# Optimization experiments

Hardware: AMD Instinct MI355X
Metric: run time of the kernel (lower is better)

## Reference

```python
import jax, jax.numpy as jnp
import numpy as np

N, E = 50000, 800000
IN_DIM, C = 128, 32
H_STD, H_REP = 3, 1
EE_HID, EE_OUT = 32, 16
NEG_SLOPE = 0.2


def setup_inputs() -> dict:
    key = jax.random.key(0)
    ks = jax.random.split(key, 24)
    rn = lambda k, shape, scale: jax.random.normal(k, shape, jnp.float32) * scale
    inp = {
        "x": rn(ks[0], (N, IN_DIM), 1.0),
        "edge_features_raw": jax.random.uniform(ks[1], (E, 7), jnp.float32),
        "edge_index": jax.random.randint(ks[2], (2, E), 0, N, dtype=jnp.int32),
        "same_type_mask": jax.random.randint(ks[3], (E,), 0, 2, dtype=jnp.int32) > 0,
        # edge encoder MLP 7 -> 32 -> 16
        "ee_w1": rn(ks[4], (7, EE_HID), 7 ** -0.5),
        "ee_b1": jnp.zeros((EE_HID,), jnp.float32),
        "ee_w2": rn(ks[5], (EE_HID, EE_OUT), EE_HID ** -0.5),
        "ee_b2": jnp.zeros((EE_OUT,), jnp.float32),
        # standard GATv2 (3 heads)
        "wl_s": rn(ks[6], (IN_DIM, H_STD * C), IN_DIM ** -0.5),
        "bl_s": jnp.zeros((H_STD * C,), jnp.float32),
        "wr_s": rn(ks[7], (IN_DIM, H_STD * C), IN_DIM ** -0.5),
        "br_s": jnp.zeros((H_STD * C,), jnp.float32),
        "we_s": rn(ks[8], (EE_OUT, H_STD * C), EE_OUT ** -0.5),
        "att_s": rn(ks[9], (H_STD, C), C ** -0.5),
        "bias_s": jnp.zeros((H_STD * C,), jnp.float32),
        # repulsion GATv2 (1 head)
        "wl_r": rn(ks[10], (IN_DIM, H_REP * C), IN_DIM ** -0.5),
        "bl_r": jnp.zeros((H_REP * C,), jnp.float32),
        "wr_r": rn(ks[11], (IN_DIM, H_REP * C), IN_DIM ** -0.5),
        "br_r": jnp.zeros((H_REP * C,), jnp.float32),
        "we_r": rn(ks[12], (EE_OUT, H_REP * C), EE_OUT ** -0.5),
        "att_r": rn(ks[13], (H_REP, C), C ** -0.5),
        "bias_r": jnp.zeros((H_REP * C,), jnp.float32),
    }
    return inp


def _gatv2(x, src, dst, edge_attr, edge_mask, wl, bl, wr, br, we, att, bias, n, h, c):
    """GATv2Conv (eval mode). src/dst already include self loops; edge_mask masks
    attention (-inf) for edges excluded from this head's graph."""
    xl = (x @ wl + bl).reshape(n, h, c)            # source transform
    xr = (x @ wr + br).reshape(n, h, c)            # target transform
    ef = (edge_attr @ we).reshape(-1, h, c)        # edge transform
    msg = xl[src] + xr[dst] + ef                   # [E', H, C]
    score = jnp.einsum('ehc,hc->eh', jax.nn.leaky_relu(msg, NEG_SLOPE), att)
    score = jnp.where(edge_mask[:, None], score, -jnp.inf)
    smax = jax.ops.segment_max(score, dst, num_segments=n)   # every node has a self loop
    a = jnp.exp(score - smax[dst])                 # masked edges -> 0
    denom = jax.ops.segment_sum(a, dst, num_segments=n)
    a = a / denom[dst]
    out = jax.ops.segment_sum(a[:, :, None] * xl[src], dst, num_segments=n)
    return out.reshape(n, h * c) + bias


def reference(x, edge_features_raw, ee_w1, ee_b1, ee_w2, ee_b2,
              wl_s, bl_s, wr_s, br_s, we_s, att_s, bias_s,
              wl_r, bl_r, wr_r, br_r, we_r, att_r, bias_r,
              edge_index, same_type_mask):
    n = x.shape[0]
    # edge encoder MLP
    ea = jax.nn.relu(edge_features_raw @ ee_w1 + ee_b1) @ ee_w2 + ee_b2  # [E, 16]
    src, dst = edge_index[0], edge_index[1]
    loop = jnp.arange(n, dtype=src.dtype)
    src_f = jnp.concatenate([src, loop])
    dst_f = jnp.concatenate([dst, loop])
    # standard conv: self-loop edge_attr = mean over all edges
    ea_std = jnp.concatenate([ea, jnp.broadcast_to(ea.mean(0), (n, ea.shape[1]))], 0)
    mask_std = jnp.ones(src_f.shape[0], bool)
    h_std = _gatv2(x, src_f, dst_f, ea_std, mask_std,
                   wl_s, bl_s, wr_s, br_s, we_s, att_s, bias_s, n, H_STD, C)
    # repulsion conv on same-type edge subset (+ self loops); loop attr = masked mean
    m = same_type_mask.astype(ea.dtype)
    ea_loop_rep = (ea * m[:, None]).sum(0) / jnp.maximum(m.sum(), 1.0)
    ea_rep = jnp.concatenate([ea, jnp.broadcast_to(ea_loop_rep, (n, ea.shape[1]))], 0)
    mask_rep = jnp.concatenate([same_type_mask, jnp.ones(n, bool)])
    h_rep = _gatv2(x, src_f, dst_f, ea_rep, mask_rep,
                   wl_r, bl_r, wr_r, br_r, we_r, att_r, bias_r, n, H_REP, C)
    return jnp.concatenate([h_std, h_rep], axis=-1)  # [N, (3+1)*32]
```

## Files before the change

### kernel.cpp

```cpp
#include <hip/hip_runtime.h>
#include <hip/hip_bf16.h>
#include <cstdint>

#define IN_DIM 128
#define OUT_STD 96
#define OUT_REP 32
#define OUT_ALL 128
#define NEG_SLOPE 0.2f
#define EE_BLOCKS 512
#define LOG2E 1.4426950408889634f

typedef _Float16 h2 __attribute__((ext_vector_type(2)));
typedef _Float16 f16x8 __attribute__((ext_vector_type(8)));
typedef float f32x4 __attribute__((ext_vector_type(4)));

template <int CTRL>
__device__ __forceinline__ float dpp_add(float v)
{
    int x = __builtin_amdgcn_update_dpp(0, __float_as_int(v), CTRL, 0xf, 0xf, true);
    return v + __int_as_float(x);
}
__device__ __forceinline__ float grp32_sum(float v)
{
    v = dpp_add<0xB1>(v);
    v = dpp_add<0x4E>(v);
    v = dpp_add<0x141>(v);
    v = dpp_add<0x140>(v);
    int x = __builtin_amdgcn_ds_swizzle(__float_as_int(v), 0x401F);
    return v + __int_as_float(x);
}

__device__ __forceinline__ int detect_mask_fl(const void* mraw, int nprobe, int* sfl)
{
    int t = threadIdx.x;
    const unsigned char* mb = (const unsigned char*)mraw;
    int anyGT1 = 0, any123 = 0;
    for (int i = t; i < nprobe; i += 256) {
        unsigned char b = mb[i];
        if (b > 1) anyGT1 = 1;
        if ((i & 3) && b) any123 = 1;
    }
    anyGT1 = __any(anyGT1);
    any123 = __any(any123);
    if (t == 0) *sfl = 0;
    __syncthreads();
    if ((t & 63) == 0) atomicOr(sfl, (anyGT1 ? 2 : 0) | (any123 ? 1 : 0));
    __syncthreads();
    int v = *sfl;
    return (v & 2) ? 2 : ((v & 1) ? 0 : 1);
}

__device__ __forceinline__ bool mask_at(const void* m, int fl, int e)
{
    if (fl == 1) return ((const int*)m)[e] != 0;
    if (fl == 2) return ((const float*)m)[e] != 0.f;
    return ((const unsigned char*)m)[e] != 0;
}

__global__ __launch_bounds__(256) void initpack(
    const float* __restrict__ wls, const float* __restrict__ wrs,
    const float* __restrict__ wlr, const float* __restrict__ wrr,
    const float* __restrict__ bls, const float* __restrict__ brs,
    const float* __restrict__ blr, const float* __restrict__ brr,
    int* __restrict__ deg, float* __restrict__ sums,
    _Float16* __restrict__ Wh, float* __restrict__ biasp, int N)
{
    int gid = blockIdx.x * 256 + threadIdx.x;
    int gs = gridDim.x * 256;
    for (int i = gid; i < N; i += gs) deg[i] = 0;
    if (gid < 64) sums[gid] = 0.f;
    for (int i = gid; i < 128 * 256; i += gs) {
        int j = i & 255, k = i >> 8;
        float v;
        if (j < 96)       v = wls[k * 96 + j];
        else if (j < 128) v = wlr[k * 32 + (j - 96)];
        else if (j < 224) v = wrs[k * 96 + (j - 128)];
        else              v = wrr[k * 32 + (j - 224)];
        Wh[j * 128 + k] = (_Float16)v;
    }
    if (gid < 256) {
        float b;
        if (gid < 96)       b = bls[gid];
        else if (gid < 128) b = blr[gid - 96];
        else if (gid < 224) b = brs[gid - 128];
        else                b = brr[gid - 224];
        biasp[gid] = b;
    }
}

__global__ __launch_bounds__(256) void edge_enc(
    const float* __restrict__ raw, const int* __restrict__ ei,
    const void* __restrict__ mraw, int nprobe,
    const float* __restrict__ w1, const float* __restrict__ b1,
    const float* __restrict__ w2, const float* __restrict__ b2,
    _Float16* __restrict__ ea, int* __restrict__ deg, float* __restrict__ sums, int E)
{
    __shared__ float sW1[224];
    __shared__ float sB1[32];
    __shared__ float sW2[512];
    __shared__ float sB2[16];
    __shared__ float sraw[256 * 7];
    __shared__ float red[33][4];
    __shared__ int sfl;
    int t = threadIdx.x;
    int fl = detect_mask_fl(mraw, nprobe, &sfl);
    if (t < 224) sW1[t] = w1[t];
    if (t < 32)  sB1[t] = b1[t];
    for (int i = t; i < 512; i += 256) sW2[i] = w2[i];
    if (t < 16)  sB2[t] = b2[t];
    __syncthreads();

    float accs[16], accm[16], cnt = 0.f;
#pragma unroll
    for (int j = 0; j < 16; ++j) { accs[j] = 0.f; accm[j] = 0.f; }

    for (int base = blockIdx.x * 256; base < E; base += gridDim.x * 256) {
        int nh = E - base; if (nh > 256) nh = 256;
        __syncthreads();
        for (int i = t; i < nh * 7; i += 256) sraw[i] = raw[(size_t)base * 7 + i];
        __syncthreads();
        int e = base + t;
        if (e < E) {
            float r[7];
#pragma unroll
            for (int k = 0; k < 7; ++k) r[k] = sraw[t * 7 + k];
            float o[16];
#pragma unroll
            for (int j = 0; j < 16; ++j) o[j] = sB2[j];
#pragma unroll
            for (int jh = 0; jh < 32; ++jh) {
                float hv = sB1[jh];
#pragma unroll
                for (int k = 0; k < 7; ++k) hv += r[k] * sW1[k * 32 + jh];
                hv = hv > 0.f ? hv : 0.f;
#pragma unroll
                for (int j = 0; j < 16; ++j) o[j] += hv * sW2[jh * 16 + j];
            }
            union { h2 h[8]; uint4 u[2]; } pk;
#pragma unroll
            for (int j = 0; j < 8; ++j) pk.h[j] = h2{(_Float16)o[2 * j], (_Float16)o[2 * j + 1]};
            uint4* dst = (uint4*)(ea + (size_t)e * 16);
            dst[0] = pk.u[0];
            dst[1] = pk.u[1];
            atomicAdd(&deg[ei[E + e]], 1);
            float mk = mask_at(mraw, fl, e) ? 1.f : 0.f;
#pragma unroll
            for (int j = 0; j < 16; ++j) { accs[j] += o[j]; accm[j] += o[j] * mk; }
            cnt += mk;
        }
    }

    int wv = t >> 6, ln = t & 63;
#pragma unroll
    for (int j = 0; j < 16; ++j) {
        float v = accs[j], vm = accm[j];
#pragma unroll
        for (int off = 32; off; off >>= 1) {
            v  += __shfl_xor(v, off, 64);
            vm += __shfl_xor(vm, off, 64);
        }
        if (ln == 0) { red[j][wv] = v; red[16 + j][wv] = vm; }
    }
    {
        float c = cnt;
#pragma unroll
        for (int off = 32; off; off >>= 1) c += __shfl_xor(c, off, 64);
        if (ln == 0) red[32][wv] = c;
    }
    __syncthreads();
    if (t < 33) {
        float v = red[t][0] + red[t][1] + red[t][2] + red[t][3];
        atomicAdd(&sums[t], v);
    }
}

__global__ __launch_bounds__(256) void scan1(const int* __restrict__ deg, int* __restrict__ part, int n)
{
    __shared__ int sm[256];
    int i = blockIdx.x * 256 + threadIdx.x;
    sm[threadIdx.x] = (i < n) ? deg[i] : 0;
    __syncthreads();
    for (int s = 128; s; s >>= 1) {
        if (threadIdx.x < s) sm[threadIdx.x] += sm[threadIdx.x + s];
        __syncthreads();
    }
    if (threadIdx.x == 0) part[blockIdx.x] = sm[0];
}

__global__ __launch_bounds__(256) void scan23p(
    const int* __restrict__ deg, const int* __restrict__ part,
    int* __restrict__ row_ofs, int* __restrict__ cursor,
    int n, int E,
    const float* __restrict__ we_s, const float* __restrict__ we_r,
    const float* __restrict__ att_s, const float* __restrict__ att_r,
    const float* __restrict__ bias_s, const float* __restrict__ bias_r,
    const float* __restrict__ sums,
    _Float16* __restrict__ wpk, float* __restrict__ eflv,
    float* __restrict__ attvv, float* __restrict__ biasvv)
{
    __shared__ int sm[256];
    __shared__ int spre;
    int t = threadIdx.x, b = blockIdx.x;
    sm[t] = (t < b) ? part[t] : 0;
    __syncthreads();
    for (int s = 128; s; s >>= 1) {
        if (t < s) sm[t] += sm[t + s];
        __syncthreads();
    }
    if (t == 0) spre = sm[0];
    __syncthreads();
    int prefix = spre;
    __syncthreads();
    int i = b * 256 + t;
    int v = (i < n) ? deg[i] : 0;
    sm[t] = v;
    __syncthreads();
    for (int o = 1; o < 256; o <<= 1) {
        int add = (t >= o) ? sm[t - o] : 0;
        __syncthreads();
        sm[t] += add;
        __syncthreads();
    }
    int excl = sm[t] - v + prefix;
    if (i < n) { row_ofs[i] = excl; cursor[i] = excl; }
    if (b == 0 && t == 0) row_ofs[n] = E;

    if (b == 0 && t < 128) {
        bool is_std = t < OUT_STD;
        int fc = is_std ? t : (t - OUT_STD);
        const float* wsrc = is_std ? we_s : we_r;
        int ldw = is_std ? OUT_STD : OUT_REP;
        const float* sp = is_std ? sums : (sums + 16);
        float c = sums[32]; c = c < 1.f ? 1.f : c;
        float scl = is_std ? (1.f / (float)E) : (1.f / c);
        float efl = 0.f;
#pragma unroll
        for (int k = 0; k < 16; ++k) {
            float v2 = wsrc[k * ldw + fc];
            wpk[t * 16 + k] = (_Float16)v2;
            efl += sp[k] * scl * v2;
        }
        eflv[t] = efl;
        attvv[t] = (is_std ? att_s[t] : att_r[fc]) * LOG2E;
        biasvv[t] = is_std ? bias_s[t] : bias_r[fc];
    }
}

__global__ __launch_bounds__(256) void csr_fill(const int* __restrict__ ei, int* __restrict__ cursor,
                                                const void* __restrict__ mraw, int nprobe,
                                                uint2* __restrict__ csr, int E)
{
    __shared__ int sfl;
    int fl = detect_mask_fl(mraw, nprobe, &sfl);
    int e = blockIdx.x * 256 + threadIdx.x;
    if (e < E) {
        int s = ei[e];
        int d = ei[E + e];
        int slot = atomicAdd(&cursor[d], 1);
        unsigned int v = (unsigned int)e;
        if (mask_at(mraw, fl, e)) v |= 0x80000000u;
        csr[slot] = make_uint2(v, (unsigned int)s);
    }
}

#define NG_BM 64
__global__ __launch_bounds__(256) void node_gemm(
    const float* __restrict__ x, const _Float16* __restrict__ Wh,
    const float* __restrict__ biasp,
    _Float16* __restrict__ XLh, float* __restrict__ XR, int n)
{
    __shared__ __align__(16) _Float16 Ash[64 * 128];
    __shared__ __align__(16) _Float16 Bsh[256 * 128];
    __shared__ float bsh[256];
    int tid = threadIdx.x;
    int m0 = blockIdx.x * NG_BM;

    bsh[tid] = biasp[tid];

    for (int c = tid; c < 64 * 16; c += 256) {
        int row = c >> 4, kc = c & 15;
        int gr = m0 + row;
        float4 a0 = make_float4(0.f, 0.f, 0.f, 0.f), a1 = a0;
        if (gr < n) {
            const float4* xp = (const float4*)(x + (size_t)gr * 128 + kc * 8);
            a0 = xp[0]; a1 = xp[1];
        }
        _Float16* dst = Ash + row * 128 + (kc ^ (row & 7)) * 8;
        dst[0] = (_Float16)a0.x; dst[1] = (_Float16)a0.y;
        dst[2] = (_Float16)a0.z; dst[3] = (_Float16)a0.w;
        dst[4] = (_Float16)a1.x; dst[5] = (_Float16)a1.y;
        dst[6] = (_Float16)a1.z; dst[7] = (_Float16)a1.w;
    }
    for (int c = tid; c < 256 * 16; c += 256) {
        int col = c >> 4, kc = c & 15;
        uint4 v = *(const uint4*)(Wh + col * 128 + kc * 8);
        *(uint4*)(Bsh + col * 128 + (kc ^ (col & 7)) * 8) = v;
    }
    __syncthreads();

    int wave = tid >> 6;
    int lane = tid & 63;
    int l16  = lane & 15;
    int lk   = lane >> 4;

    f32x4 acc0, acc1, acc2, acc3, acc4, acc5, acc6, acc7;
    f32x4 acc8, acc9, acc10, acc11, acc12, acc13, acc14, acc15;
    acc0 = acc1 = acc2 = acc3 = acc4 = acc5 = acc6 = acc7 = f32x4{0.f, 0.f, 0.f, 0.f};
    acc8 = acc9 = acc10 = acc11 = acc12 = acc13 = acc14 = acc15 = f32x4{0.f, 0.f, 0.f, 0.f};

#pragma unroll
    for (int kk = 0; kk < 4; ++kk) {
        int arow = wave * 16 + l16;
        f16x8 afrag = *(const f16x8*)(Ash + arow * 128 + ((kk * 4 + lk) ^ (arow & 7)) * 8);
#define BF(nt) (*(const f16x8*)(Bsh + (nt * 16 + l16) * 128 + ((kk * 4 + lk) ^ ((nt * 16 + l16) & 7)) * 8))
        acc0  = __builtin_amdgcn_mfma_f32_16x16x32_f16(afrag, BF(0),  acc0,  0, 0, 0);
        acc1  = __builtin_amdgcn_mfma_f32_16x16x32_f16(afrag, BF(1),  acc1,  0, 0, 0);
        acc2  = __builtin_amdgcn_mfma_f32_16x16x32_f16(afrag, BF(2),  acc2,  0, 0, 0);
        acc3  = __builtin_amdgcn_mfma_f32_16x16x32_f16(afrag, BF(3),  acc3,  0, 0, 0);
        acc4  = __builtin_amdgcn_mfma_f32_16x16x32_f16(afrag, BF(4),  acc4,  0, 0, 0);
        acc5  = __builtin_amdgcn_mfma_f32_16x16x32_f16(afrag, BF(5),  acc5,  0, 0, 0);
        acc6  = __builtin_amdgcn_mfma_f32_16x16x32_f16(afrag, BF(6),  acc6,  0, 0, 0);
        acc7  = __builtin_amdgcn_mfma_f32_16x16x32_f16(afrag, BF(7),  acc7,  0, 0, 0);
        acc8  = __builtin_amdgcn_mfma_f32_16x16x32_f16(afrag, BF(8),  acc8,  0, 0, 0);
        acc9  = __builtin_amdgcn_mfma_f32_16x16x32_f16(afrag, BF(9),  acc9,  0, 0, 0);
        acc10 = __builtin_amdgcn_mfma_f32_16x16x32_f16(afrag, BF(10), acc10, 0, 0, 0);
        acc11 = __builtin_amdgcn_mfma_f32_16x16x32_f16(afrag, BF(11), acc11, 0, 0, 0);
        acc12 = __builtin_amdgcn_mfma_f32_16x16x32_f16(afrag, BF(12), acc12, 0, 0, 0);
        acc13 = __builtin_amdgcn_mfma_f32_16x16x32_f16(afrag, BF(13), acc13, 0, 0, 0);
        acc14 = __builtin_amdgcn_mfma_f32_16x16x32_f16(afrag, BF(14), acc14, 0, 0, 0);
        acc15 = __builtin_amdgcn_mfma_f32_16x16x32_f16(afrag, BF(15), acc15, 0, 0, 0);
#undef BF
    }

#define STORE_ACC(nt, accv)                                             \
    {                                                                   \
        int col = nt * 16 + l16;                                        \
        float bv = bsh[col];                                            \
        _Pragma("unroll")                                               \
        for (int r = 0; r < 4; ++r) {                                   \
            int row = m0 + wave * 16 + lk * 4 + r;                      \
            if (row < n) {                                              \
                float v = accv[r] + bv;                                 \
                if (col < 128) XLh[(size_t)row * 128 + col] = (_Float16)v; \
                else           XR[(size_t)row * 128 + (col - 128)] = v; \
            }                                                           \
        }                                                               \
    }
    STORE_ACC(0, acc0)   STORE_ACC(1, acc1)   STORE_ACC(2, acc2)   STORE_ACC(3, acc3)
    STORE_ACC(4, acc4)   STORE_ACC(5, acc5)   STORE_ACC(6, acc6)   STORE_ACC(7, acc7)
    STORE_ACC(8, acc8)   STORE_ACC(9, acc9)   STORE_ACC(10, acc10) STORE_ACC(11, acc11)
    STORE_ACC(12, acc12) STORE_ACC(13, acc13) STORE_ACC(14, acc14) STORE_ACC(15, acc15)
#undef STORE_ACC
}

__device__ __forceinline__ void edge_sc(
    const _Float16* __restrict__ XLh, const _Float16* __restrict__ ea,
    const uint2* __restrict__ csr, int pp, int f, bool is_std,
    float xr_n, float attv,
    h2 w0, h2 w1, h2 w2, h2 w3, h2 w4, h2 w5, h2 w6, h2 w7,
    float& s, float& x)
{
    uint2 pk = csr[pp];
    int e = __builtin_amdgcn_readfirstlane((int)(pk.x & 0x7fffffffu));
    bool act = is_std || (pk.x & 0x80000000u);
    int src = __builtin_amdgcn_readfirstlane((int)pk.y);
    x = (float)XLh[(size_t)src * 128 + f];
    union { uint4 u[2]; h2 h[8]; } pe;
    const uint4* eap = (const uint4*)(ea + (size_t)e * 16);
    pe.u[0] = eap[0]; pe.u[1] = eap[1];
    float efv = x + xr_n;
    efv = __builtin_amdgcn_fdot2(pe.h[0], w0, efv, false);
    efv = __builtin_amdgcn_fdot2(pe.h[1], w1, efv, false);
    efv = __builtin_amdgcn_fdot2(pe.h[2], w2, efv, false);
    efv = __builtin_amdgcn_fdot2(pe.h[3], w3, efv, false);
    efv = __builtin_amdgcn_fdot2(pe.h[4], w4, efv, false);
    efv = __builtin_amdgcn_fdot2(pe.h[5], w5, efv, false);
    efv = __builtin_amdgcn_fdot2(pe.h[6], w6, efv, false);
    efv = __builtin_amdgcn_fdot2(pe.h[7], w7, efv, false);
    float lk = fmaxf(efv, NEG_SLOPE * efv);
    float sv = grp32_sum(lk * attv);
    s = act ? sv : -INFINITY;
}

__global__ __launch_bounds__(128, 4) void gat_main(
    const _Float16* __restrict__ XLh, const float* __restrict__ XR,
    const _Float16* __restrict__ ea, const uint2* __restrict__ csr,
    const int* __restrict__ row_ofs,
    const _Float16* __restrict__ wpk, const float* __restrict__ eflv,
    const float* __restrict__ attvv, const float* __restrict__ biasvv,
    float* __restrict__ out, int n)
{
    int node = blockIdx.x;
    int f = threadIdx.x;
    bool is_std = f < OUT_STD;

    union { uint4 u; h2 h[4]; } c0, c1;
    const uint4* wp = (const uint4*)(wpk + (size_t)f * 16);
    c0.u = wp[0]; c1.u = wp[1];
    h2 w0 = c0.h[0], w1 = c0.h[1], w2 = c0.h[2], w3 = c0.h[3];
    h2 w4 = c1.h[0], w5 = c1.h[1], w6 = c1.h[2], w7 = c1.h[3];

    float efl   = eflv[f];
    float attv  = attvv[f];
    float biasv = biasvv[f];

    float xl_n = (float)XLh[(size_t)node * 128 + f];
    float xr_n = XR[(size_t)node * 128 + f];

    float msg = xl_n + xr_n + efl;
    float lk0 = fmaxf(msg, NEG_SLOPE * msg);
    float m = grp32_sum(lk0 * attv);
    float denom = 1.f, acc = xl_n;

    int p0 = row_ofs[node], p1 = row_ofs[node + 1];
    int p = p0;
    for (; p + 8 <= p1; p += 8) {
        float s0, s1, s2, s3, s4, s5, s6, s7;
        float x0, x1, x2, x3, x4, x5, x6, x7;
        edge_sc(XLh, ea, csr, p + 0, f, is_std, xr_n, attv, w0, w1, w2, w3, w4, w5, w6, w7, s0, x0);
        edge_sc(XLh, ea, csr, p + 1, f, is_std, xr_n, attv, w0, w1, w2, w3, w4, w5, w6, w7, s1, x1);
        edge_sc(XLh, ea, csr, p + 2, f, is_std, xr_n, attv, w0, w1, w2, w3, w4, w5, w6, w7, s2, x2);
        edge_sc(XLh, ea, csr, p + 3, f, is_std, xr_n, attv, w0, w1, w2, w3, w4, w5, w6, w7, s3, x3);
        edge_sc(XLh, ea, csr, p + 4, f, is_std, xr_n, attv, w0, w1, w2, w3, w4, w5, w6, w7, s4, x4);
        edge_sc(XLh, ea, csr, p + 5, f, is_std, xr_n, attv, w0, w1, w2, w3, w4, w5, w6, w7, s5, x5);
        edge_sc(XLh, ea, csr, p + 6, f, is_std, xr_n, attv, w0, w1, w2, w3, w4, w5, w6, w7, s6, x6);
        edge_sc(XLh, ea, csr, p + 7, f, is_std, xr_n, attv, w0, w1, w2, w3, w4, w5, w6, w7, s7, x7);

        float mn = fmaxf(m, fmaxf(fmaxf(fmaxf(s0, s1), fmaxf(s2, s3)),
                                  fmaxf(fmaxf(s4, s5), fmaxf(s6, s7))));
        float r  = exp2f(m - mn);
        float q0 = exp2f(s0 - mn), q1 = exp2f(s1 - mn);
        float q2 = exp2f(s2 - mn), q3 = exp2f(s3 - mn);
        float q4 = exp2f(s4 - mn), q5 = exp2f(s5 - mn);
        float q6 = exp2f(s6 - mn), q7 = exp2f(s7 - mn);
        denom = denom * r + (((q0 + q1) + (q2 + q3)) + ((q4 + q5) + (q6 + q7)));
        acc   = acc * r + (((q0 * x0 + q1 * x1) + (q2 * x2 + q3 * x3))
                         + ((q4 * x4 + q5 * x5) + (q6 * x6 + q7 * x7)));
        m = mn;
    }
    for (; p < p1; ++p) {
        float s8, x8;
        edge_sc(XLh, ea, csr, p, f, is_std, xr_n, attv, w0, w1, w2, w3, w4, w5, w6, w7, s8, x8);
        float mn = fmaxf(m, s8);
        float r  = exp2f(m - mn);
        float q  = exp2f(s8 - mn);
        denom = denom * r + q;
        acc   = acc * r + q * x8;
        m = mn;
    }
    out[(size_t)node * OUT_ALL + f] = acc / denom + biasv;
}

extern "C" void kernel_launch(void* const* d_in, const int* in_sizes, int n_in,
                              void* d_out, int out_size, void* d_ws, size_t ws_size,
                              hipStream_t stream)
{
    const float* x    = (const float*)d_in[0];
    const float* raw  = (const float*)d_in[1];
    const int*   ei   = (const int*)d_in[2];
    const void*  mask_raw = d_in[3];
    const float* ee_w1 = (const float*)d_in[4];
    const float* ee_b1 = (const float*)d_in[5];
    const float* ee_w2 = (const float*)d_in[6];
    const float* ee_b2 = (const float*)d_in[7];
    const float* wl_s = (const float*)d_in[8];
    const float* bl_s = (const float*)d_in[9];
    const float* wr_s = (const float*)d_in[10];
    const float* br_s = (const float*)d_in[11];
    const float* we_s = (const float*)d_in[12];
    const float* att_s = (const float*)d_in[13];
    const float* bias_s = (const float*)d_in[14];
    const float* wl_r = (const float*)d_in[15];
    const float* bl_r = (const float*)d_in[16];
    const float* wr_r = (const float*)d_in[17];
    const float* br_r = (const float*)d_in[18];
    const float* we_r = (const float*)d_in[19];
    const float* att_r = (const float*)d_in[20];
    const float* bias_r = (const float*)d_in[21];

    const int N = in_sizes[0] / IN_DIM;
    const int E = in_sizes[1] / 7;

    char* w = (char*)d_ws;
    size_t off = 0;
    auto carve = [&](size_t bytes) {
        void* p = w + off;
        off = (off + bytes + 255) & ~(size_t)255;
        return p;
    };
    _Float16* XLh  = (_Float16*)carve((size_t)N * 128 * 2);
    float* XR      = (float*)carve((size_t)N * 128 * 4);
    _Float16* ea   = (_Float16*)carve((size_t)E * 16 * 2);
    uint2* csr     = (uint2*)carve((size_t)E * 8);
    int*   row_ofs = (int*)carve((size_t)(N + 1) * 4);
    int*   cursor  = (int*)carve((size_t)N * 4);
    int*   deg     = (int*)carve((size_t)N * 4);
    int*   part    = (int*)carve(1024);
    float* sums    = (float*)carve(256);
    _Float16* Wh   = (_Float16*)carve((size_t)256 * 128 * 2);
    float* biasp   = (float*)carve(1024);
    _Float16* wpk  = (_Float16*)carve((size_t)128 * 16 * 2);
    float* eflv    = (float*)carve(512);
    float* attvv   = (float*)carve(512);
    float* biasvv  = (float*)carve(512);
    (void)ws_size; (void)n_in; (void)out_size;

    int ebl = (E + 255) / 256;
    int nbl = (N + 255) / 256;
    int nprobe = E < 4096 ? E : 4096;
    int eebl = ebl < EE_BLOCKS ? ebl : EE_BLOCKS;

    initpack<<<160, 256, 0, stream>>>(wl_s, wr_s, wl_r, wr_r, bl_s, br_s, bl_r, br_r,
                                      deg, sums, Wh, biasp, N);
    edge_enc<<<eebl, 256, 0, stream>>>(raw, ei, mask_raw, nprobe,
                                       ee_w1, ee_b1, ee_w2, ee_b2, ea, deg, sums, E);
    scan1<<<nbl, 256, 0, stream>>>(deg, part, N);
    scan23p<<<nbl, 256, 0, stream>>>(deg, part, row_ofs, cursor, N, E,
                                     we_s, we_r, att_s, att_r, bias_s, bias_r, sums,
                                     wpk, eflv, attvv, biasvv);
    csr_fill<<<ebl, 256, 0, stream>>>(ei, cursor, mask_raw, nprobe, csr, E);
    node_gemm<<<(N + NG_BM - 1) / NG_BM, 256, 0, stream>>>(x, Wh, biasp, XLh, XR, N);
    gat_main<<<N, 128, 0, stream>>>(XLh, XR, ea, csr, row_ofs,
                                    wpk, eflv, attvv, biasvv,
                                    (float*)d_out, N);
}
```

Baseline: 285.4 us.

## Fuse edge encoder and node GEMM into one launch; grid-stride GAT kernel

The edge encoder and node GEMM become one kernel whose block index picks the role, so the two independent stages run at the same time and one launch is saved. The combined kernel always declares an 80 KB shared buffer, which can limit occupancy for the edge-encoder blocks. Separately, gat_main now launches at most 4096 blocks that loop over nodes with a grid stride, instead of one block per node. This cuts block scheduling overhead but may reduce latency hiding or load balance across nodes.

```diff
diff --git a/kernel.cpp b/kernel.cpp
--- a/kernel.cpp
+++ b/kernel.cpp
@@ -9,6 +9,7 @@
 #define NEG_SLOPE 0.2f
 #define EE_BLOCKS 512
 #define LOG2E 1.4426950408889634f
+#define NG_BM 64
 
 typedef _Float16 h2 __attribute__((ext_vector_type(2)));
 typedef _Float16 f16x8 __attribute__((ext_vector_type(8)));
@@ -88,196 +89,107 @@
     }
 }
 
-__global__ __launch_bounds__(256) void edge_enc(
+__global__ __launch_bounds__(256) void ee_gemm(
     const float* __restrict__ raw, const int* __restrict__ ei,
     const void* __restrict__ mraw, int nprobe,
     const float* __restrict__ w1, const float* __restrict__ b1,
     const float* __restrict__ w2, const float* __restrict__ b2,
-    _Float16* __restrict__ ea, int* __restrict__ deg, float* __restrict__ sums, int E)
-{
-    __shared__ float sW1[224];
-    __shared__ float sB1[32];
-    __shared__ float sW2[512];
-    __shared__ float sB2[16];
-    __shared__ float sraw[256 * 7];
-    __shared__ float red[33][4];
-    __shared__ int sfl;
-    int t = threadIdx.x;
-    int fl = detect_mask_fl(mraw, nprobe, &sfl);
-    if (t < 224) sW1[t] = w1[t];
-    if (t < 32)  sB1[t] = b1[t];
-    for (int i = t; i < 512; i += 256) sW2[i] = w2[i];
-    if (t < 16)  sB2[t] = b2[t];
-    __syncthreads();
-
-    float accs[16], accm[16], cnt = 0.f;
-#pragma unroll
-    for (int j = 0; j < 16; ++j) { accs[j] = 0.f; accm[j] = 0.f; }
-
-    for (int base = blockIdx.x * 256; base < E; base += gridDim.x * 256) {
-        int nh = E - base; if (nh > 256) nh = 256;
-        __syncthreads();
-        for (int i = t; i < nh * 7; i += 256) sraw[i] = raw[(size_t)base * 7 + i];
-        __syncthreads();
-        int e = base + t;
-        if (e < E) {
-            float r[7];
-#pragma unroll
-            for (int k = 0; k < 7; ++k) r[k] = sraw[t * 7 + k];
-            float o[16];
-#pragma unroll
-            for (int j = 0; j < 16; ++j) o[j] = sB2[j];
-#pragma unroll
-            for (int jh = 0; jh < 32; ++jh) {
-                float hv = sB1[jh];
-#pragma unroll
-                for (int k = 0; k < 7; ++k) hv += r[k] * sW1[k * 32 + jh];
-                hv = hv > 0.f ? hv : 0.f;
-#pragma unroll
-                for (int j = 0; j < 16; ++j) o[j] += hv * sW2[jh * 16 + j];
-            }
-            union { h2 h[8]; uint4 u[2]; } pk;
-#pragma unroll
-            for (int j = 0; j < 8; ++j) pk.h[j] = h2{(_Float16)o[2 * j], (_Float16)o[2 * j + 1]};
-            uint4* dst = (uint4*)(ea + (size_t)e * 16);
-            dst[0] = pk.u[0];
-            dst[1] = pk.u[1];
-            atomicAdd(&deg[ei[E + e]], 1);
-            float mk = mask_at(mraw, fl, e) ? 1.f : 0.f;
-#pragma unroll
-            for (int j = 0; j < 16; ++j) { accs[j] += o[j]; accm[j] += o[j] * mk; }
-            cnt += mk;
-        }
-    }
-
-    int wv = t >> 6, ln = t & 63;
-#pragma unroll
-    for (int j = 0; j < 16; ++j) {
-        float v = accs[j], vm = accm[j];
-#pragma unroll
-        for (int off = 32; off; off >>= 1) {
-            v  += __shfl_xor(v, off, 64);
-            vm += __shfl_xor(vm, off, 64);
-        }
-        if (ln == 0) { red[j][wv] = v; red[16 + j][wv] = vm; }
-    }
-    {
-        float c = cnt;
-#pragma unroll
-        for (int off = 32; off; off >>= 1) c += __shfl_xor(c, off, 64);
-        if (ln == 0) red[32][wv] = c;
-    }
-    __syncthreads();
-    if (t < 33) {
-        float v = red[t][0] + red[t][1] + red[t][2] + red[t][3];
-        atomicAdd(&sums[t], v);
-    }
-}
-
-__global__ __launch_bounds__(256) void scan1(const int* __restrict__ deg, int* __restrict__ part, int n)
-{
-    __shared__ int sm[256];
-    int i = blockIdx.x * 256 + threadIdx.x;
-    sm[threadIdx.x] = (i < n) ? deg[i] : 0;
-    __syncthreads();
-    for (int s = 128; s; s >>= 1) {
-        if (threadIdx.x < s) sm[threadIdx.x] += sm[threadIdx.x + s];
-        __syncthreads();
-    }
-    if (threadIdx.x == 0) part[blockIdx.x] = sm[0];
-}
-
-__global__ __launch_bounds__(256) void scan23p(
-    const int* __restrict__ deg, const int* __restrict__ part,
-    int* __restrict__ row_ofs, int* __restrict__ cursor,
-    int n, int E,
-    const float* __restrict__ we_s, const float* __restrict__ we_r,
-    const float* __restrict__ att_s, const float* __restrict__ att_r,
-    const float* __restrict__ bias_s, const float* __restrict__ bias_r,
-    const float* __restrict__ sums,
-    _Float16* __restrict__ wpk, float* __restrict__ eflv,
-    float* __restrict__ attvv, float* __restrict__ biasvv)
-{
-    __shared__ int sm[256];
-    __shared__ int spre;
-    int t = threadIdx.x, b = blockIdx.x;
-    sm[t] = (t < b) ? part[t] : 0;
-    __syncthreads();
-    for (int s = 128; s; s >>= 1) {
-        if (t < s) sm[t] += sm[t + s];
-        __syncthreads();
-    }
-    if (t == 0) spre = sm[0];
-    __syncthreads();
-    int prefix = spre;
-    __syncthreads();
-    int i = b * 256 + t;
-    int v = (i < n) ? deg[i] : 0;
-    sm[t] = v;
-    __syncthreads();
-    for (int o = 1; o < 256; o <<= 1) {
-        int add = (t >= o) ? sm[t - o] : 0;
-        __syncthreads();
-        sm[t] += add;
-        __syncthreads();
-    }
-    int excl = sm[t] - v + prefix;
-    if (i < n) { row_ofs[i] = excl; cursor[i] = excl; }
-    if (b == 0 && t == 0) row_ofs[n] = E;
-
-    if (b == 0 && t < 128) {
-        bool is_std = t < OUT_STD;
-        int fc = is_std ? t : (t - OUT_STD);
-        const float* wsrc = is_std ? we_s : we_r;
-        int ldw = is_std ? OUT_STD : OUT_REP;
-        const float* sp = is_std ? sums : (sums + 16);
-        float c = sums[32]; c = c < 1.f ? 1.f : c;
-        float scl = is_std ? (1.f / (float)E) : (1.f / c);
-        float efl = 0.f;
-#pragma unroll
-        for (int k = 0; k < 16; ++k) {
-            float v2 = wsrc[k * ldw + fc];
-            wpk[t * 16 + k] = (_Float16)v2;
-            efl += sp[k] * scl * v2;
-        }
-        eflv[t] = efl;
-        attvv[t] = (is_std ? att_s[t] : att_r[fc]) * LOG2E;
-        biasvv[t] = is_std ? bias_s[t] : bias_r[fc];
-    }
-}
-
-__global__ __launch_bounds__(256) void csr_fill(const int* __restrict__ ei, int* __restrict__ cursor,
-                                                const void* __restrict__ mraw, int nprobe,
-                                                uint2* __restrict__ csr, int E)
-{
-    __shared__ int sfl;
-    int fl = detect_mask_fl(mraw, nprobe, &sfl);
-    int e = blockIdx.x * 256 + threadIdx.x;
-    if (e < E) {
-        int s = ei[e];
-        int d = ei[E + e];
-        int slot = atomicAdd(&cursor[d], 1);
-        unsigned int v = (unsigned int)e;
-        if (mask_at(mraw, fl, e)) v |= 0x80000000u;
-        csr[slot] = make_uint2(v, (unsigned int)s);
-    }
-}
-
-#define NG_BM 64
-__global__ __launch_bounds__(256) void node_gemm(
+    _Float16* __restrict__ ea, int* __restrict__ deg, float* __restrict__ sums,
+    int E, int eebl,
     const float* __restrict__ x, const _Float16* __restrict__ Wh,
     const float* __restrict__ biasp,
     _Float16* __restrict__ XLh, float* __restrict__ XR, int n)
 {
-    __shared__ __align__(16) _Float16 Ash[64 * 128];
-    __shared__ __align__(16) _Float16 Bsh[256 * 128];
-    __shared__ float bsh[256];
-    int tid = threadIdx.x;
-    int m0 = blockIdx.x * NG_BM;
-
-    bsh[tid] = biasp[tid];
-
-    for (int c = tid; c < 64 * 16; c += 256) {
+    __shared__ __align__(16) unsigned char lds[80 * 1024];
+    int t = threadIdx.x;
+
+    if (blockIdx.x < eebl) {
+        float* sW1  = (float*)lds;
+        float* sB1  = sW1 + 224;
+        float* sW2  = sB1 + 32;
+        float* sB2  = sW2 + 512;
+        float* sraw = sB2 + 16;
+        float (*red)[4] = (float(*)[4])(sraw + 1792);
+        int* sfl = (int*)(red + 33);
+
+        int fl = detect_mask_fl(mraw, nprobe, sfl);
+        if (t < 224) sW1[t] = w1[t];
+        if (t < 32)  sB1[t] = b1[t];
+        for (int i = t; i < 512; i += 256) sW2[i] = w2[i];
+        if (t < 16)  sB2[t] = b2[t];
+        __syncthreads();
+
+        float accs[16], accm[16], cnt = 0.f;
+#pragma unroll
+        for (int j = 0; j < 16; ++j) { accs[j] = 0.f; accm[j] = 0.f; }
+
+        int gstride = eebl * 256;
+        for (int base = blockIdx.x * 256; base < E; base += gstride) {
+            int nh = E - base; if (nh > 256) nh = 256;
+            __syncthreads();
+            for (int i = t; i < nh * 7; i += 256) sraw[i] = raw[(size_t)base * 7 + i];
+            __syncthreads();
+            int e = base + t;
+            if (e < E) {
+                float r[7];
+#pragma unroll
+                for (int k = 0; k < 7; ++k) r[k] = sraw[t * 7 + k];
+                float o[16];
+#pragma unroll
+                for (int j = 0; j < 16; ++j) o[j] = sB2[j];
+#pragma unroll
+                for (int jh = 0; jh < 32; ++jh) {
+                    float hv = sB1[jh];
+#pragma unroll
+                    for (int k = 0; k < 7; ++k) hv += r[k] * sW1[k * 32 + jh];
+                    hv = hv > 0.f ? hv : 0.f;
+#pragma unroll
+                    for (int j = 0; j < 16; ++j) o[j] += hv * sW2[jh * 16 + j];
+                }
+                union { h2 h[8]; uint4 u[2]; } pk;
+#pragma unroll
+                for (int j = 0; j < 8; ++j) pk.h[j] = h2{(_Float16)o[2 * j], (_Float16)o[2 * j + 1]};
+                uint4* dst = (uint4*)(ea + (size_t)e * 16);
+                dst[0] = pk.u[0];
+                dst[1] = pk.u[1];
+                atomicAdd(&deg[ei[E + e]], 1);
+                float mk = mask_at(mraw, fl, e) ? 1.f : 0.f;
+#pragma unroll
+                for (int j = 0; j < 16; ++j) { accs[j] += o[j]; accm[j] += o[j] * mk; }
+                cnt += mk;
+            }
+        }
+
+        int wv = t >> 6, ln = t & 63;
+#pragma unroll
+        for (int j = 0; j < 16; ++j) {
+            float v = accs[j], vm = accm[j];
+#pragma unroll
+            for (int off = 32; off; off >>= 1) {
+                v  += __shfl_xor(v, off, 64);
+                vm += __shfl_xor(vm, off, 64);
+            }
+            if (ln == 0) { red[j][wv] = v; red[16 + j][wv] = vm; }
+        }
+        {
+            float c = cnt;
+#pragma unroll
+            for (int off = 32; off; off >>= 1) c += __shfl_xor(c, off, 64);
+            if (ln == 0) red[32][wv] = c;
+        }
+        __syncthreads();
+        if (t < 33) {
+            float v = red[t][0] + red[t][1] + red[t][2] + red[t][3];
+            atomicAdd(&sums[t], v);
+        }
+        return;
+    }
+
+    _Float16* Ash = (_Float16*)lds;
+    _Float16* Bsh = Ash + 64 * 128;
+    int m0 = (blockIdx.x - eebl) * NG_BM;
+
+    for (int c = t; c < 64 * 16; c += 256) {
         int row = c >> 4, kc = c & 15;
         int gr = m0 + row;
         float4 a0 = make_float4(0.f, 0.f, 0.f, 0.f), a1 = a0;
@@ -291,15 +203,15 @@
         dst[4] = (_Float16)a1.x; dst[5] = (_Float16)a1.y;
         dst[6] = (_Float16)a1.z; dst[7] = (_Float16)a1.w;
     }
-    for (int c = tid; c < 256 * 16; c += 256) {
+    for (int c = t; c < 256 * 16; c += 256) {
         int col = c >> 4, kc = c & 15;
         uint4 v = *(const uint4*)(Wh + col * 128 + kc * 8);
         *(uint4*)(Bsh + col * 128 + (kc ^ (col & 7)) * 8) = v;
     }
     __syncthreads();
 
-    int wave = tid >> 6;
-    int lane = tid & 63;
+    int wave = t >> 6;
+    int lane = t & 63;
     int l16  = lane & 15;
     int lk   = lane >> 4;
 
@@ -335,7 +247,7 @@
 #define STORE_ACC(nt, accv)                                             \
     {                                                                   \
         int col = nt * 16 + l16;                                        \
-        float bv = bsh[col];                                            \
+        float bv = biasp[col];                                          \
         _Pragma("unroll")                                               \
         for (int r = 0; r < 4; ++r) {                                   \
             int row = m0 + wave * 16 + lk * 4 + r;                      \
@@ -351,6 +263,95 @@
     STORE_ACC(8, acc8)   STORE_ACC(9, acc9)   STORE_ACC(10, acc10) STORE_ACC(11, acc11)
     STORE_ACC(12, acc12) STORE_ACC(13, acc13) STORE_ACC(14, acc14) STORE_ACC(15, acc15)
 #undef STORE_ACC
+}
+
+__global__ __launch_bounds__(256) void scan1(const int* __restrict__ deg, int* __restrict__ part, int n)
+{
+    __shared__ int sm[256];
+    int i = blockIdx.x * 256 + threadIdx.x;
+    sm[threadIdx.x] = (i < n) ? deg[i] : 0;
+    __syncthreads();
+    for (int s = 128; s; s >>= 1) {
+        if (threadIdx.x < s) sm[threadIdx.x] += sm[threadIdx.x + s];
+        __syncthreads();
+    }
+    if (threadIdx.x == 0) part[blockIdx.x] = sm[0];
+}
+
+__global__ __launch_bounds__(256) void scan23p(
+    const int* __restrict__ deg, const int* __restrict__ part,
+    int* __restrict__ row_ofs, int* __restrict__ cursor,
+    int n, int E,
+    const float* __restrict__ we_s, const float* __restrict__ we_r,
+    const float* __restrict__ att_s, const float* __restrict__ att_r,
+    const float* __restrict__ bias_s, const float* __restrict__ bias_r,
+    const float* __restrict__ sums,
+    _Float16* __restrict__ wpk, float* __restrict__ eflv,
+    float* __restrict__ attvv, float* __restrict__ biasvv)
+{
+    __shared__ int sm[256];
+    __shared__ int spre;
+    int t = threadIdx.x, b = blockIdx.x;
+    sm[t] = (t < b) ? part[t] : 0;
+    __syncthreads();
+    for (int s = 128; s; s >>= 1) {
+        if (t < s) sm[t] += sm[t + s];
+        __syncthreads();
+    }
+    if (t == 0) spre = sm[0];
+    __syncthreads();
+    int prefix = spre;
+    __syncthreads();
+    int i = b * 256 + t;
+    int v = (i < n) ? deg[i] : 0;
+    sm[t] = v;
+    __syncthreads();
+    for (int o = 1; o < 256; o <<= 1) {
+        int add = (t >= o) ? sm[t - o] : 0;
+        __syncthreads();
+        sm[t] += add;
+        __syncthreads();
+    }
+    int excl = sm[t] - v + prefix;
+    if (i < n) { row_ofs[i] = excl; cursor[i] = excl; }
+    if (b == 0 && t == 0) row_ofs[n] = E;
+
+    if (b == 0 && t < 128) {
+        bool is_std = t < OUT_STD;
+        int fc = is_std ? t : (t - OUT_STD);
+        const float* wsrc = is_std ? we_s : we_r;
+        int ldw = is_std ? OUT_STD : OUT_REP;
+        const float* sp = is_std ? sums : (sums + 16);
+        float c = sums[32]; c = c < 1.f ? 1.f : c;
+        float scl = is_std ? (1.f / (float)E) : (1.f / c);
+        float efl = 0.f;
+#pragma unroll
+        for (int k = 0; k < 16; ++k) {
+            float v2 = wsrc[k * ldw + fc];
+            wpk[t * 16 + k] = (_Float16)v2;
+            efl += sp[k] * scl * v2;
+        }
+        eflv[t] = efl;
+        attvv[t] = (is_std ? att_s[t] : att_r[fc]) * LOG2E;
+        biasvv[t] = is_std ? bias_s[t] : bias_r[fc];
+    }
+}
+
+__global__ __launch_bounds__(256) void csr_fill(const int* __restrict__ ei, int* __restrict__ cursor,
+                                                const void* __restrict__ mraw, int nprobe,
+                                                uint2* __restrict__ csr, int E)
+{
+    __shared__ int sfl;
+    int fl = detect_mask_fl(mraw, nprobe, &sfl);
+    int e = blockIdx.x * 256 + threadIdx.x;
+    if (e < E) {
+        int s = ei[e];
+        int d = ei[E + e];
+        int slot = atomicAdd(&cursor[d], 1);
+        unsigned int v = (unsigned int)e;
+        if (mask_at(mraw, fl, e)) v |= 0x80000000u;
+        csr[slot] = make_uint2(v, (unsigned int)s);
+    }
 }
 
 __device__ __forceinline__ void edge_sc(
@@ -390,7 +391,6 @@
     const float* __restrict__ attvv, const float* __restrict__ biasvv,
     float* __restrict__ out, int n)
 {
-    int node = blockIdx.x;
     int f = threadIdx.x;
     bool is_std = f < OUT_STD;
 
@@ -404,51 +404,53 @@
     float attv  = attvv[f];
     float biasv = biasvv[f];
 
-    float xl_n = (float)XLh[(size_t)node * 128 + f];
-    float xr_n = XR[(size_t)node * 128 + f];
-
-    float msg = xl_n + xr_n + efl;
-    float lk0 = fmaxf(msg, NEG_SLOPE * msg);
-    float m = grp32_sum(lk0 * attv);
-    float denom = 1.f, acc = xl_n;
-
-    int p0 = row_ofs[node], p1 = row_ofs[node + 1];
-    int p = p0;
-    for (; p + 8 <= p1; p += 8) {
-        float s0, s1, s2, s3, s4, s5, s6, s7;
-        float x0, x1, x2, x3, x4, x5, x6, x7;
-        edge_sc(XLh, ea, csr, p + 0, f, is_std, xr_n, attv, w0, w1, w2, w3, w4, w5, w6, w7, s0, x0);
-        edge_sc(XLh, ea, csr, p + 1, f, is_std, xr_n, attv, w0, w1, w2, w3, w4, w5, w6, w7, s1, x1);
-        edge_sc(XLh, ea, csr, p + 2, f, is_std, xr_n, attv, w0, w1, w2, w3, w4, w5, w6, w7, s2, x2);
-        edge_sc(XLh, ea, csr, p + 3, f, is_std, xr_n, attv, w0, w1, w2, w3, w4, w5, w6, w7, s3, x3);
-        edge_sc(XLh, ea, csr, p + 4, f, is_std, xr_n, attv, w0, w1, w2, w3, w4, w5, w6, w7, s4, x4);
-        edge_sc(XLh, ea, csr, p + 5, f, is_std, xr_n, attv, w0, w1, w2, w3, w4, w5, w6, w7, s5, x5);
-        edge_sc(XLh, ea, csr, p + 6, f, is_std, xr_n, attv, w0, w1, w2, w3, w4, w5, w6, w7, s6, x6);
-        edge_sc(XLh, ea, csr, p + 7, f, is_std, xr_n, attv, w0, w1, w2, w3, w4, w5, w6, w7, s7, x7);
-
-        float mn = fmaxf(m, fmaxf(fmaxf(fmaxf(s0, s1), fmaxf(s2, s3)),
-                                  fmaxf(fmaxf(s4, s5), fmaxf(s6, s7))));
-        float r  = exp2f(m - mn);
-        float q0 = exp2f(s0 - mn), q1 = exp2f(s1 - mn);
-        float q2 = exp2f(s2 - mn), q3 = exp2f(s3 - mn);
-        float q4 = exp2f(s4 - mn), q5 = exp2f(s5 - mn);
-        float q6 = exp2f(s6 - mn), q7 = exp2f(s7 - mn);
-        denom = denom * r + (((q0 + q1) + (q2 + q3)) + ((q4 + q5) + (q6 + q7)));
-        acc   = acc * r + (((q0 * x0 + q1 * x1) + (q2 * x2 + q3 * x3))
-                         + ((q4 * x4 + q5 * x5) + (q6 * x6 + q7 * x7)));
-        m = mn;
-    }
-    for (; p < p1; ++p) {
-        float s8, x8;
-        edge_sc(XLh, ea, csr, p, f, is_std, xr_n, attv, w0, w1, w2, w3, w4, w5, w6, w7, s8, x8);
-        float mn = fmaxf(m, s8);
-        float r  = exp2f(m - mn);
-        float q  = exp2f(s8 - mn);
-        denom = denom * r + q;
-        acc   = acc * r + q * x8;
-        m = mn;
-    }
-    out[(size_t)node * OUT_ALL + f] = acc / denom + biasv;
+    for (int node = blockIdx.x; node < n; node += gridDim.x) {
+        float xl_n = (float)XLh[(size_t)node * 128 + f];
+        float xr_n = XR[(size_t)node * 128 + f];
+
+        float msg = xl_n + xr_n + efl;
+        float lk0 = fmaxf(msg, NEG_SLOPE * msg);
+        float m = grp32_sum(lk0 * attv);
+        float denom = 1.f, acc = xl_n;
+
+        int p0 = row_ofs[node], p1 = row_ofs[node + 1];
+        int p = p0;
+        for (; p + 8 <= p1; p += 8) {
+            float s0, s1, s2, s3, s4, s5, s6, s7;
+            float x0, x1, x2, x3, x4, x5, x6, x7;
+            edge_sc(XLh, ea, csr, p + 0, f, is_std, xr_n, attv, w0, w1, w2, w3, w4, w5, w6, w7, s0, x0);
+            edge_sc(XLh, ea, csr, p + 1, f, is_std, xr_n, attv, w0, w1, w2, w3, w4, w5, w6, w7, s1, x1);
+            edge_sc(XLh, ea, csr, p + 2, f, is_std, xr_n, attv, w0, w1, w2, w3, w4, w5, w6, w7, s2, x2);
+            edge_sc(XLh, ea, csr, p + 3, f, is_std, xr_n, attv, w0, w1, w2, w3, w4, w5, w6, w7, s3, x3);
+            edge_sc(XLh, ea, csr, p + 4, f, is_std, xr_n, attv, w0, w1, w2, w3, w4, w5, w6, w7, s4, x4);
+            edge_sc(XLh, ea, csr, p + 5, f, is_std, xr_n, attv, w0, w1, w2, w3, w4, w5, w6, w7, s5, x5);
+            edge_sc(XLh, ea, csr, p + 6, f, is_std, xr_n, attv, w0, w1, w2, w3, w4, w5, w6, w7, s6, x6);
+            edge_sc(XLh, ea, csr, p + 7, f, is_std, xr_n, attv, w0, w1, w2, w3, w4, w5, w6, w7, s7, x7);
+
+            float mn = fmaxf(m, fmaxf(fmaxf(fmaxf(s0, s1), fmaxf(s2, s3)),
+                                      fmaxf(fmaxf(s4, s5), fmaxf(s6, s7))));
+            float r  = exp2f(m - mn);
+            float q0 = exp2f(s0 - mn), q1 = exp2f(s1 - mn);
+            float q2 = exp2f(s2 - mn), q3 = exp2f(s3 - mn);
+            float q4 = exp2f(s4 - mn), q5 = exp2f(s5 - mn);
+            float q6 = exp2f(s6 - mn), q7 = exp2f(s7 - mn);
+            denom = denom * r + (((q0 + q1) + (q2 + q3)) + ((q4 + q5) + (q6 + q7)));
+            acc   = acc * r + (((q0 * x0 + q1 * x1) + (q2 * x2 + q3 * x3))
+                             + ((q4 * x4 + q5 * x5) + (q6 * x6 + q7 * x7)));
+            m = mn;
+        }
+        for (; p < p1; ++p) {
+            float s8, x8;
+            edge_sc(XLh, ea, csr, p, f, is_std, xr_n, attv, w0, w1, w2, w3, w4, w5, w6, w7, s8, x8);
+            float mn = fmaxf(m, s8);
+            float r  = exp2f(m - mn);
+            float q  = exp2f(s8 - mn);
+            denom = denom * r + q;
+            acc   = acc * r + q * x8;
+            m = mn;
+        }
+        out[(size_t)node * OUT_ALL + f] = acc / denom + biasv;
+    }
 }
 
 extern "C" void kernel_launch(void* const* d_in, const int* in_sizes, int n_in,
@@ -509,18 +511,20 @@
     int nbl = (N + 255) / 256;
     int nprobe = E < 4096 ? E : 4096;
     int eebl = ebl < EE_BLOCKS ? ebl : EE_BLOCKS;
+    int ngbl = (N + NG_BM - 1) / NG_BM;
 
     initpack<<<160, 256, 0, stream>>>(wl_s, wr_s, wl_r, wr_r, bl_s, br_s, bl_r, br_r,
                                       deg, sums, Wh, biasp, N);
-    edge_enc<<<eebl, 256, 0, stream>>>(raw, ei, mask_raw, nprobe,
-                                       ee_w1, ee_b1, ee_w2, ee_b2, ea, deg, sums, E);
+    ee_gemm<<<eebl + ngbl, 256, 0, stream>>>(raw, ei, mask_raw, nprobe,
+                                             ee_w1, ee_b1, ee_w2, ee_b2, ea, deg, sums, E, eebl,
+                                             x, Wh, biasp, XLh, XR, N);
     scan1<<<nbl, 256, 0, stream>>>(deg, part, N);
     scan23p<<<nbl, 256, 0, stream>>>(deg, part, row_ofs, cursor, N, E,
                                      we_s, we_r, att_s, att_r, bias_s, bias_r, sums,
                                      wpk, eflv, attvv, biasvv);
     csr_fill<<<ebl, 256, 0, stream>>>(ei, cursor, mask_raw, nprobe, csr, E);
-    node_gemm<<<(N + NG_BM - 1) / NG_BM, 256, 0, stream>>>(x, Wh, biasp, XLh, XR, N);
-    gat_main<<<N, 128, 0, stream>>>(XLh, XR, ea, csr, row_ofs,
-                                    wpk, eflv, attvv, biasvv,
-                                    (float*)d_out, N);
-}
+    int gat_blocks = N < 4096 ? N : 4096;
+    gat_main<<<gat_blocks, 128, 0, stream>>>(XLh, XR, ea, csr, row_ofs,
+                                             wpk, eflv, attvv, biasvv,
+                                             (float*)d_out, N);
+}
```

After: 341.7 us. 19.7% more time.
